# Optimization experiments

Measured on AMD Instinct MI355X. Metric: run time of the kernel, lower is better.

The kernel has to match this reference:

```python
import jax, jax.numpy as jnp
import numpy as np

NUM_NODES = 200000
EMB_DIM = 64
NUM_EDGES = 6400000
NUM_LAYERS = 4


def setup_inputs() -> dict:
    key = jax.random.key(0)
    k1, k2, k3, k4 = jax.random.split(key, 4)
    embeds = jax.random.normal(k1, (NUM_NODES, EMB_DIM), dtype=jnp.float32)
    adj_rows = jax.random.randint(k2, (NUM_EDGES,), 0, NUM_NODES, dtype=jnp.int64)
    adj_cols = jax.random.randint(k3, (NUM_EDGES,), 0, NUM_NODES, dtype=jnp.int64)
    adj_vals = jax.random.uniform(k4, (NUM_EDGES,), dtype=jnp.float32)
    return {"embeds": embeds, "adj_rows": adj_rows, "adj_cols": adj_cols, "adj_vals": adj_vals}


def _spmm(rows, cols, vals, x):
    # Sparse (COO) adjacency @ dense x: out[r] += v * x[c]
    msgs = vals[:, None] * x[cols]  # [E, d] gather + scale
    return jax.ops.segment_sum(msgs, rows, num_segments=NUM_NODES)


def reference(embeds, adj_rows, adj_cols, adj_vals):
    x = embeds
    acc = x  # running sum over layer outputs (fuses stack+mean)
    for _ in range(NUM_LAYERS):
        x = _spmm(adj_rows, adj_cols, adj_vals, x)
        acc = acc + x
    return acc / jnp.float32(NUM_LAYERS + 1)
```

## Files before the change

### kernel.cpp

```cpp
#include <hip/hip_runtime.h>

#define N_NODES 200000
#define DIM 64
#define BSHIFT 9
#define NB 391
#define NB_PAD 512
#define CHUNK 4096

__device__ __forceinline__ float bf2f(unsigned short u) {
    return __uint_as_float(((unsigned int)u) << 16);
}
__device__ __forceinline__ unsigned short f2bf(float f) {
    unsigned int u = __float_as_uint(f);
    u += 0x7FFFu + ((u >> 16) & 1u);
    return (unsigned short)(u >> 16);
}

__global__ __launch_bounds__(256) void bucket_hist(const int* __restrict__ rows, int E,
                                                   int* __restrict__ bcnt) {
    __shared__ int h[NB_PAD];
    for (int i = threadIdx.x; i < NB_PAD; i += 256) h[i] = 0;
    __syncthreads();
    int stride = gridDim.x * blockDim.x;
    for (int e = blockIdx.x * blockDim.x + threadIdx.x; e < E; e += stride)
        atomicAdd(&h[rows[e] >> BSHIFT], 1);
    __syncthreads();
    for (int i = threadIdx.x; i < NB; i += 256)
        if (h[i]) atomicAdd(&bcnt[i], h[i]);
}

__global__ void bucket_scan(const int* __restrict__ bcnt, int* __restrict__ bbase,
                            int* __restrict__ bcur) {
    if (threadIdx.x == 0 && blockIdx.x == 0) {
        int run = 0;
        for (int i = 0; i < NB; i++) { bbase[i] = run; bcur[i] = run; run += bcnt[i]; }
        bbase[NB] = run;
    }
}

__global__ __launch_bounds__(256) void bucket_scatter(const int* __restrict__ rows,
                                                      const int* __restrict__ cols,
                                                      const float* __restrict__ vals, int E,
                                                      int* __restrict__ bcur,
                                                      int2* __restrict__ tmp) {
    __shared__ int h[NB_PAD];
    __shared__ int incl[NB_PAD];
    __shared__ int sbuf[NB_PAD];
    __shared__ int fix[NB_PAD];
    __shared__ int cur2[NB_PAD];
    __shared__ int2 stage[CHUNK];
    __shared__ unsigned short sbkt[CHUNK];
    const int base = blockIdx.x * CHUNK;
    const int count = min(CHUNK, E - base);
    const int t = threadIdx.x;

    for (int i = t; i < NB_PAD; i += 256) h[i] = 0;
    __syncthreads();
    for (int i = t; i < count; i += 256)
        atomicAdd(&h[rows[base + i] >> BSHIFT], 1);
    __syncthreads();
    for (int i = t; i < NB_PAD; i += 256) incl[i] = h[i];
    __syncthreads();
    for (int off = 1; off < NB_PAD; off <<= 1) {
        for (int i = t; i < NB_PAD; i += 256)
            sbuf[i] = incl[i] + ((i >= off) ? incl[i - off] : 0);
        __syncthreads();
        for (int i = t; i < NB_PAD; i += 256) incl[i] = sbuf[i];
        __syncthreads();
    }
    for (int i = t; i < NB; i += 256) {
        int excl = incl[i] - h[i];
        int g = h[i] ? atomicAdd(&bcur[i], h[i]) : 0;
        fix[i] = g - excl;
        cur2[i] = excl;
    }
    __syncthreads();
    for (int i = t; i < count; i += 256) {
        int r = rows[base + i];
        int b = r >> BSHIFT;
        int slot = atomicAdd(&cur2[b], 1);
        int key = ((r & ((1 << BSHIFT) - 1)) << 18) | cols[base + i];
        stage[slot] = make_int2(key, __float_as_int(vals[base + i]));
        sbkt[slot] = (unsigned short)b;
    }
    __syncthreads();
    for (int s = t; s < count; s += 256)
        tmp[s + fix[sbkt[s]]] = stage[s];
}

__global__ __launch_bounds__(256) void bucket_sort(const int2* __restrict__ tmp,
                                                   const int* __restrict__ bbase,
                                                   int2* __restrict__ sorted,
                                                   int* __restrict__ row_start) {
    __shared__ int h[NB_PAD];
    __shared__ int sums[256];
    const int b = blockIdx.x;
    const int s0 = bbase[b], s1 = bbase[b + 1];
    const int t = threadIdx.x;
    h[t] = 0; h[t + 256] = 0;
    __syncthreads();
    for (int e = s0 + t; e < s1; e += 256)
        atomicAdd(&h[tmp[e].x >> 18], 1);
    __syncthreads();
    int a0 = h[2 * t], a1 = h[2 * t + 1];
    sums[t] = a0 + a1;
    __syncthreads();
    if (t == 0) {
        int run = 0;
        for (int i = 0; i < 256; i++) { int v = sums[i]; sums[i] = run; run += v; }
    }
    __syncthreads();
    int e0 = sums[t];
    h[2 * t] = e0;
    h[2 * t + 1] = e0 + a0;
    __syncthreads();
    int rbase = b << BSHIFT;
    for (int r = t; r < (1 << BSHIFT); r += 256) {
        int row = rbase + r;
        if (row < N_NODES) row_start[row] = s0 + h[r];
    }
    if (b == NB - 1 && t == 0) row_start[N_NODES] = s1;
    __syncthreads();
    for (int e = s0 + t; e < s1; e += 256) {
        int2 kv = tmp[e];
        int r = kv.x >> 18;
        int rank = atomicAdd(&h[r], 1);
        sorted[s0 + rank] = make_int2(kv.x & 0x3FFFF, kv.y);
    }
}

__global__ __launch_bounds__(256) void convert_kernel(const float* __restrict__ src,
                                                      unsigned short* __restrict__ dst, int n4) {
    int i = blockIdx.x * blockDim.x + threadIdx.x;
    if (i >= n4) return;
    float4 v = *(const float4*)(src + i * 4);
    ushort4 o;
    o.x = f2bf(v.x); o.y = f2bf(v.y); o.z = f2bf(v.z); o.w = f2bf(v.w);
    *(ushort4*)(dst + i * 4) = o;
}

template <int MODE>
__global__ __launch_bounds__(256) void spmm_kernel(const int2* __restrict__ sorted,
                                                   const int* __restrict__ row_start,
                                                   const unsigned short* __restrict__ xb,
                                                   const float* __restrict__ embeds,
                                                   unsigned short* __restrict__ y,
                                                   float* __restrict__ acc) {
    int gid = blockIdx.x * blockDim.x + threadIdx.x;
    int r = gid >> 4;
    if (r >= N_NODES) return;
    int j = (gid & 15) << 2;
    int e = row_start[r], eend = row_start[r + 1];
    float4 a = make_float4(0.f, 0.f, 0.f, 0.f);
    for (; e + 4 <= eend; e += 4) {
        int2 c0 = sorted[e];
        int2 c1 = sorted[e + 1];
        int2 c2 = sorted[e + 2];
        int2 c3 = sorted[e + 3];
        ushort4 u0 = *(const ushort4*)(xb + (c0.x << 6) + j);
        ushort4 u1 = *(const ushort4*)(xb + (c1.x << 6) + j);
        ushort4 u2 = *(const ushort4*)(xb + (c2.x << 6) + j);
        ushort4 u3 = *(const ushort4*)(xb + (c3.x << 6) + j);
        float v0 = __int_as_float(c0.y), v1 = __int_as_float(c1.y);
        float v2 = __int_as_float(c2.y), v3 = __int_as_float(c3.y);
        a.x = fmaf(v0, bf2f(u0.x), a.x); a.y = fmaf(v0, bf2f(u0.y), a.y);
        a.z = fmaf(v0, bf2f(u0.z), a.z); a.w = fmaf(v0, bf2f(u0.w), a.w);
        a.x = fmaf(v1, bf2f(u1.x), a.x); a.y = fmaf(v1, bf2f(u1.y), a.y);
        a.z = fmaf(v1, bf2f(u1.z), a.z); a.w = fmaf(v1, bf2f(u1.w), a.w);
        a.x = fmaf(v2, bf2f(u2.x), a.x); a.y = fmaf(v2, bf2f(u2.y), a.y);
        a.z = fmaf(v2, bf2f(u2.z), a.z); a.w = fmaf(v2, bf2f(u2.w), a.w);
        a.x = fmaf(v3, bf2f(u3.x), a.x); a.y = fmaf(v3, bf2f(u3.y), a.y);
        a.z = fmaf(v3, bf2f(u3.z), a.z); a.w = fmaf(v3, bf2f(u3.w), a.w);
    }
    for (; e < eend; ++e) {
        int2 cv = sorted[e];
        ushort4 u = *(const ushort4*)(xb + (cv.x << 6) + j);
        float v = __int_as_float(cv.y);
        a.x = fmaf(v, bf2f(u.x), a.x);
        a.y = fmaf(v, bf2f(u.y), a.y);
        a.z = fmaf(v, bf2f(u.z), a.z);
        a.w = fmaf(v, bf2f(u.w), a.w);
    }
    int o = (r << 6) + j;
    if (MODE == 0) {
        ushort4 yo; yo.x = f2bf(a.x); yo.y = f2bf(a.y); yo.z = f2bf(a.z); yo.w = f2bf(a.w);
        *(ushort4*)(y + o) = yo;
        const float4 x0 = *(const float4*)(embeds + o);
        *(float4*)(acc + o) = make_float4(x0.x + a.x, x0.y + a.y, x0.z + a.z, x0.w + a.w);
    } else if (MODE == 1) {
        ushort4 yo; yo.x = f2bf(a.x); yo.y = f2bf(a.y); yo.z = f2bf(a.z); yo.w = f2bf(a.w);
        *(ushort4*)(y + o) = yo;
        float4 c = *(const float4*)(acc + o);
        *(float4*)(acc + o) = make_float4(c.x + a.x, c.y + a.y, c.z + a.z, c.w + a.w);
    } else {
        float4 c = *(const float4*)(acc + o);
        const float s = 0.2f;
        *(float4*)(acc + o) = make_float4((c.x + a.x) * s, (c.y + a.y) * s,
                                          (c.z + a.z) * s, (c.w + a.w) * s);
    }
}

extern "C" void kernel_launch(void* const* d_in, const int* in_sizes, int n_in,
                              void* d_out, int out_size, void* d_ws, size_t ws_size,
                              hipStream_t stream) {
    const float* embeds = (const float*)d_in[0];
    const int*   rows   = (const int*)d_in[1];
    const int*   cols   = (const int*)d_in[2];
    const float* vals   = (const float*)d_in[3];
    float* acc = (float*)d_out;
    const int E = in_sizes[1];

    char* ws = (char*)d_ws;
    size_t off = 0;
    auto alloc = [&](size_t bytes) -> char* {
        char* p = ws + off;
        off = (off + bytes + 255) & ~(size_t)255;
        return p;
    };
    int*   bcnt      = (int*)alloc((size_t)NB * 4);
    int*   bbase     = (int*)alloc((size_t)(NB + 1) * 4);
    int*   bcur      = (int*)alloc((size_t)NB * 4);
    int*   row_start = (int*)alloc((size_t)(N_NODES + 1) * 4);
    int2*  sorted    = (int2*)alloc((size_t)E * 8);
    unsigned short* xb0 = (unsigned short*)alloc((size_t)N_NODES * DIM * 2);
    unsigned short* xb1 = (unsigned short*)alloc((size_t)N_NODES * DIM * 2);
    int2*  tmp       = (int2*)alloc((size_t)E * 8);

    hipMemsetAsync(bcnt, 0, (size_t)NB * 4, stream);

    bucket_hist<<<512, 256, 0, stream>>>(rows, E, bcnt);
    bucket_scan<<<1, 64, 0, stream>>>(bcnt, bbase, bcur);
    bucket_scatter<<<(E + CHUNK - 1) / CHUNK, 256, 0, stream>>>(rows, cols, vals, E, bcur, tmp);
    bucket_sort<<<NB, 256, 0, stream>>>(tmp, bbase, sorted, row_start);

    int n4 = N_NODES * DIM / 4;
    convert_kernel<<<(n4 + 255) / 256, 256, 0, stream>>>(embeds, xb0, n4);

    int sb = (N_NODES * 16 + 255) / 256;
    spmm_kernel<0><<<sb, 256, 0, stream>>>(sorted, row_start, xb0, embeds, xb1, acc);
    spmm_kernel<1><<<sb, 256, 0, stream>>>(sorted, row_start, xb1, embeds, xb0, acc);
    spmm_kernel<1><<<sb, 256, 0, stream>>>(sorted, row_start, xb0, embeds, xb1, acc);
    spmm_kernel<2><<<sb, 256, 0, stream>>>(sorted, row_start, xb1, embeds, xb0, acc);
}
```

Measured before the change: 887.9 us.

## Split sorted edges into int cols and bf16 vals, defer accumulation to final layer

Sorted edge storage changes from interleaved int2 (col, fp32 val) to separate int column and bf16 value arrays, cutting edge-stream bytes per layer from 8 to 6. The per-layer fp32 acc read-modify-write is replaced by keeping each layer's bf16 output in its own buffer, with the tmp buffer reused as scratch. A final kernel sums embeds and all layer outputs once. The serial bucket scan is also replaced by a parallel shared-memory scan. This lowers precision of edge values to bf16.

New measurement: 891.8 us. Within noise of the previous version (+0.4%).

```diff
diff --git a/kernel.cpp b/kernel.cpp
--- a/kernel.cpp
+++ b/kernel.cpp
@@ -29,12 +29,25 @@
         if (h[i]) atomicAdd(&bcnt[i], h[i]);
 }
 
-__global__ void bucket_scan(const int* __restrict__ bcnt, int* __restrict__ bbase,
-                            int* __restrict__ bcur) {
-    if (threadIdx.x == 0 && blockIdx.x == 0) {
-        int run = 0;
-        for (int i = 0; i < NB; i++) { bbase[i] = run; bcur[i] = run; run += bcnt[i]; }
-        bbase[NB] = run;
+__global__ __launch_bounds__(NB_PAD) void bucket_scan(const int* __restrict__ bcnt,
+                                                      int* __restrict__ bbase,
+                                                      int* __restrict__ bcur) {
+    __shared__ int s[NB_PAD];
+    int t = threadIdx.x;
+    int mine = (t < NB) ? bcnt[t] : 0;
+    s[t] = mine;
+    __syncthreads();
+    for (int off = 1; off < NB_PAD; off <<= 1) {
+        int v = s[t] + ((t >= off) ? s[t - off] : 0);
+        __syncthreads();
+        s[t] = v;
+        __syncthreads();
+    }
+    if (t < NB) {
+        int excl = s[t] - mine;
+        bbase[t] = excl;
+        bcur[t] = excl;
+        if (t == NB - 1) bbase[NB] = s[t];
     }
 }
 
@@ -90,7 +103,8 @@
 
 __global__ __launch_bounds__(256) void bucket_sort(const int2* __restrict__ tmp,
                                                    const int* __restrict__ bbase,
-                                                   int2* __restrict__ sorted,
+                                                   int* __restrict__ cols_s,
+                                                   unsigned short* __restrict__ vals_s,
                                                    int* __restrict__ row_start) {
     __shared__ int h[NB_PAD];
     __shared__ int sums[256];
@@ -125,7 +139,9 @@
         int2 kv = tmp[e];
         int r = kv.x >> 18;
         int rank = atomicAdd(&h[r], 1);
-        sorted[s0 + rank] = make_int2(kv.x & 0x3FFFF, kv.y);
+        int pos = s0 + rank;
+        cols_s[pos] = kv.x & 0x3FFFF;
+        vals_s[pos] = f2bf(__int_as_float(kv.y));
     }
 }
 
@@ -139,30 +155,19 @@
     *(ushort4*)(dst + i * 4) = o;
 }
 
-template <int MODE>
-__global__ __launch_bounds__(256) void spmm_kernel(const int2* __restrict__ sorted,
-                                                   const int* __restrict__ row_start,
-                                                   const unsigned short* __restrict__ xb,
-                                                   const float* __restrict__ embeds,
-                                                   unsigned short* __restrict__ y,
-                                                   float* __restrict__ acc) {
-    int gid = blockIdx.x * blockDim.x + threadIdx.x;
-    int r = gid >> 4;
-    if (r >= N_NODES) return;
-    int j = (gid & 15) << 2;
-    int e = row_start[r], eend = row_start[r + 1];
+__device__ __forceinline__ float4 row_gather(const int* __restrict__ cols_s,
+                                             const unsigned short* __restrict__ vals_s,
+                                             const unsigned short* __restrict__ xb,
+                                             int e, int eend, int j) {
     float4 a = make_float4(0.f, 0.f, 0.f, 0.f);
     for (; e + 4 <= eend; e += 4) {
-        int2 c0 = sorted[e];
-        int2 c1 = sorted[e + 1];
-        int2 c2 = sorted[e + 2];
-        int2 c3 = sorted[e + 3];
-        ushort4 u0 = *(const ushort4*)(xb + (c0.x << 6) + j);
-        ushort4 u1 = *(const ushort4*)(xb + (c1.x << 6) + j);
-        ushort4 u2 = *(const ushort4*)(xb + (c2.x << 6) + j);
-        ushort4 u3 = *(const ushort4*)(xb + (c3.x << 6) + j);
-        float v0 = __int_as_float(c0.y), v1 = __int_as_float(c1.y);
-        float v2 = __int_as_float(c2.y), v3 = __int_as_float(c3.y);
+        int c0 = cols_s[e], c1 = cols_s[e + 1], c2 = cols_s[e + 2], c3 = cols_s[e + 3];
+        float v0 = bf2f(vals_s[e]),     v1 = bf2f(vals_s[e + 1]);
+        float v2 = bf2f(vals_s[e + 2]), v3 = bf2f(vals_s[e + 3]);
+        ushort4 u0 = *(const ushort4*)(xb + (c0 << 6) + j);
+        ushort4 u1 = *(const ushort4*)(xb + (c1 << 6) + j);
+        ushort4 u2 = *(const ushort4*)(xb + (c2 << 6) + j);
+        ushort4 u3 = *(const ushort4*)(xb + (c3 << 6) + j);
         a.x = fmaf(v0, bf2f(u0.x), a.x); a.y = fmaf(v0, bf2f(u0.y), a.y);
         a.z = fmaf(v0, bf2f(u0.z), a.z); a.w = fmaf(v0, bf2f(u0.w), a.w);
         a.x = fmaf(v1, bf2f(u1.x), a.x); a.y = fmaf(v1, bf2f(u1.y), a.y);
@@ -173,31 +178,56 @@
         a.z = fmaf(v3, bf2f(u3.z), a.z); a.w = fmaf(v3, bf2f(u3.w), a.w);
     }
     for (; e < eend; ++e) {
-        int2 cv = sorted[e];
-        ushort4 u = *(const ushort4*)(xb + (cv.x << 6) + j);
-        float v = __int_as_float(cv.y);
+        int c = cols_s[e];
+        float v = bf2f(vals_s[e]);
+        ushort4 u = *(const ushort4*)(xb + (c << 6) + j);
         a.x = fmaf(v, bf2f(u.x), a.x);
         a.y = fmaf(v, bf2f(u.y), a.y);
         a.z = fmaf(v, bf2f(u.z), a.z);
         a.w = fmaf(v, bf2f(u.w), a.w);
     }
+    return a;
+}
+
+__global__ __launch_bounds__(256) void spmm_prop(const int* __restrict__ cols_s,
+                                                 const unsigned short* __restrict__ vals_s,
+                                                 const int* __restrict__ row_start,
+                                                 const unsigned short* __restrict__ xb,
+                                                 unsigned short* __restrict__ y) {
+    int gid = blockIdx.x * blockDim.x + threadIdx.x;
+    int r = gid >> 4;
+    if (r >= N_NODES) return;
+    int j = (gid & 15) << 2;
+    float4 a = row_gather(cols_s, vals_s, xb, row_start[r], row_start[r + 1], j);
+    ushort4 yo; yo.x = f2bf(a.x); yo.y = f2bf(a.y); yo.z = f2bf(a.z); yo.w = f2bf(a.w);
+    *(ushort4*)(y + (r << 6) + j) = yo;
+}
+
+__global__ __launch_bounds__(256) void spmm_final(const int* __restrict__ cols_s,
+                                                  const unsigned short* __restrict__ vals_s,
+                                                  const int* __restrict__ row_start,
+                                                  const unsigned short* __restrict__ y3,
+                                                  const float* __restrict__ embeds,
+                                                  const unsigned short* __restrict__ y1,
+                                                  const unsigned short* __restrict__ y2,
+                                                  float* __restrict__ acc) {
+    int gid = blockIdx.x * blockDim.x + threadIdx.x;
+    int r = gid >> 4;
+    if (r >= N_NODES) return;
+    int j = (gid & 15) << 2;
+    float4 a = row_gather(cols_s, vals_s, y3, row_start[r], row_start[r + 1], j);
     int o = (r << 6) + j;
-    if (MODE == 0) {
-        ushort4 yo; yo.x = f2bf(a.x); yo.y = f2bf(a.y); yo.z = f2bf(a.z); yo.w = f2bf(a.w);
-        *(ushort4*)(y + o) = yo;
-        const float4 x0 = *(const float4*)(embeds + o);
-        *(float4*)(acc + o) = make_float4(x0.x + a.x, x0.y + a.y, x0.z + a.z, x0.w + a.w);
-    } else if (MODE == 1) {
-        ushort4 yo; yo.x = f2bf(a.x); yo.y = f2bf(a.y); yo.z = f2bf(a.z); yo.w = f2bf(a.w);
-        *(ushort4*)(y + o) = yo;
-        float4 c = *(const float4*)(acc + o);
-        *(float4*)(acc + o) = make_float4(c.x + a.x, c.y + a.y, c.z + a.z, c.w + a.w);
-    } else {
-        float4 c = *(const float4*)(acc + o);
-        const float s = 0.2f;
-        *(float4*)(acc + o) = make_float4((c.x + a.x) * s, (c.y + a.y) * s,
-                                          (c.z + a.z) * s, (c.w + a.w) * s);
-    }
+    const float4 e0 = *(const float4*)(embeds + o);
+    ushort4 u1 = *(const ushort4*)(y1 + o);
+    ushort4 u2 = *(const ushort4*)(y2 + o);
+    ushort4 u3 = *(const ushort4*)(y3 + o);
+    const float s = 0.2f;
+    float4 out;
+    out.x = (e0.x + bf2f(u1.x) + bf2f(u2.x) + bf2f(u3.x) + a.x) * s;
+    out.y = (e0.y + bf2f(u1.y) + bf2f(u2.y) + bf2f(u3.y) + a.y) * s;
+    out.z = (e0.z + bf2f(u1.z) + bf2f(u2.z) + bf2f(u3.z) + a.z) * s;
+    out.w = (e0.w + bf2f(u1.w) + bf2f(u2.w) + bf2f(u3.w) + a.w) * s;
+    *(float4*)(acc + o) = out;
 }
 
 extern "C" void kernel_launch(void* const* d_in, const int* in_sizes, int n_in,
@@ -221,24 +251,27 @@
     int*   bbase     = (int*)alloc((size_t)(NB + 1) * 4);
     int*   bcur      = (int*)alloc((size_t)NB * 4);
     int*   row_start = (int*)alloc((size_t)(N_NODES + 1) * 4);
-    int2*  sorted    = (int2*)alloc((size_t)E * 8);
+    int*   cols_s    = (int*)alloc((size_t)E * 4);
+    unsigned short* vals_s = (unsigned short*)alloc((size_t)E * 2);
     unsigned short* xb0 = (unsigned short*)alloc((size_t)N_NODES * DIM * 2);
-    unsigned short* xb1 = (unsigned short*)alloc((size_t)N_NODES * DIM * 2);
+    unsigned short* y1  = (unsigned short*)alloc((size_t)N_NODES * DIM * 2);
     int2*  tmp       = (int2*)alloc((size_t)E * 8);
+    unsigned short* y2 = (unsigned short*)tmp;
+    unsigned short* y3 = (unsigned short*)tmp + (size_t)N_NODES * DIM;
 
     hipMemsetAsync(bcnt, 0, (size_t)NB * 4, stream);
 
     bucket_hist<<<512, 256, 0, stream>>>(rows, E, bcnt);
-    bucket_scan<<<1, 64, 0, stream>>>(bcnt, bbase, bcur);
+    bucket_scan<<<1, NB_PAD, 0, stream>>>(bcnt, bbase, bcur);
     bucket_scatter<<<(E + CHUNK - 1) / CHUNK, 256, 0, stream>>>(rows, cols, vals, E, bcur, tmp);
-    bucket_sort<<<NB, 256, 0, stream>>>(tmp, bbase, sorted, row_start);
+    bucket_sort<<<NB, 256, 0, stream>>>(tmp, bbase, cols_s, vals_s, row_start);
 
     int n4 = N_NODES * DIM / 4;
     convert_kernel<<<(n4 + 255) / 256, 256, 0, stream>>>(embeds, xb0, n4);
 
     int sb = (N_NODES * 16 + 255) / 256;
-    spmm_kernel<0><<<sb, 256, 0, stream>>>(sorted, row_start, xb0, embeds, xb1, acc);
-    spmm_kernel<1><<<sb, 256, 0, stream>>>(sorted, row_start, xb1, embeds, xb0, acc);
-    spmm_kernel<1><<<sb, 256, 0, stream>>>(sorted, row_start, xb0, embeds, xb1, acc);
-    spmm_kernel<2><<<sb, 256, 0, stream>>>(sorted, row_start, xb1, embeds, xb0, acc);
-}
+    spmm_prop<<<sb, 256, 0, stream>>>(cols_s, vals_s, row_start, xb0, y1);
+    spmm_prop<<<sb, 256, 0, stream>>>(cols_s, vals_s, row_start, y1, y2);
+    spmm_prop<<<sb, 256, 0, stream>>>(cols_s, vals_s, row_start, y2, y3);
+    spmm_final<<<sb, 256, 0, stream>>>(cols_s, vals_s, row_start, y3, embeds, y1, y2, acc);
+}
```
